# Performance work log

Hardware: AMD Instinct MI355X
Metric: run time of the kernel (lower is better)

Reference implementation:

```python
import jax, jax.numpy as jnp
import numpy as np

N_NODES = 1_000_000
E = 262_144
N_FEAT_COLS = 9        # columns 1..9 of x
CARD = 50_000          # cardinality of each feature embedding table
EMB = 128
EDGE_DIM = 27
# node type (col 0) that activates each feature column h (h = col index - 1):
# files (type 0) use cols 1..4, processes (type 1) use col 5, sockets (type 2) use cols 6..9
TYPE_PER_COL = (0, 0, 0, 0, 1, 2, 2, 2, 2)


def setup_inputs() -> dict:
    key = jax.random.key(0)
    ks = jax.random.split(key, 10)
    type_col = jax.random.randint(ks[0], (N_NODES, 1), 0, 3, dtype=jnp.int32)
    feat_cols = jax.random.randint(ks[1], (N_NODES, N_FEAT_COLS), 0, CARD, dtype=jnp.int32)
    x = jnp.concatenate([type_col, feat_cols], axis=1)  # [N_NODES, 10]
    src = jax.random.randint(ks[2], (E,), 0, N_NODES, dtype=jnp.int32)
    dst = jax.random.randint(ks[3], (E,), 0, N_NODES, dtype=jnp.int32)
    neg_dst = jax.random.randint(ks[4], (E,), 0, N_NODES, dtype=jnp.int32)
    msg = jax.random.normal(ks[5], (E, EDGE_DIM), dtype=jnp.float32)
    emb_type = jax.random.normal(ks[6], (3, EMB), dtype=jnp.float32)            # embeddings[0]
    emb_feats = jax.random.normal(ks[7], (N_FEAT_COLS, CARD, EMB), dtype=jnp.float32)  # embeddings[1..9]
    edge_w = jax.random.normal(ks[8], (EMB, EDGE_DIM), dtype=jnp.float32) / np.sqrt(EDGE_DIM)
    edge_b = jnp.zeros((EMB,), dtype=jnp.float32)
    out_w = jax.random.normal(ks[9], (1, EMB), dtype=jnp.float32) / np.sqrt(EMB)
    out_b = jnp.zeros((1,), dtype=jnp.float32)
    return dict(x=x, src=src, dst=dst, neg_dst=neg_dst, msg=msg,
                emb_type=emb_type, emb_feats=emb_feats,
                edge_w=edge_w, edge_b=edge_b, out_w=out_w, out_b=out_b)


def _encode_features(rows, emb_type, emb_feats):
    """rows: [E,10] int. Equivalent to torch encode_features: per node type,
    sum the type-specific embedding lookups; col-0 (type) embedding is shared."""
    t = rows[:, 0]                     # [E] node type
    out = emb_type[t]                  # embeddings[0] applies to every type
    for h in range(N_FEAT_COLS):       # small fixed loop over 9 tables
        mask = (t == TYPE_PER_COL[h]).astype(out.dtype)[:, None]   # [E,1]
        out = out + emb_feats[h][rows[:, h + 1]] * mask            # masked gather-sum
    return out                         # [E, EMB]


def reference(x, src, dst, neg_dst, msg, emb_type, emb_feats, edge_w, edge_b, out_w, out_b):
    h_src = _encode_features(x[src], emb_type, emb_feats)       # [E, EMB]
    h_pos_dst = _encode_features(x[dst], emb_type, emb_feats)
    h_neg_dst = _encode_features(x[neg_dst], emb_type, emb_feats)
    target_msg = msg @ edge_w.T + edge_b                        # Linear(edge_dim -> EMB)
    h_pos_edge = jax.nn.relu(h_src + h_pos_dst)
    h_neg_edge = jax.nn.relu(h_src + h_neg_dst)
    pos = (h_pos_edge + target_msg) @ out_w.T + out_b           # [E, 1]
    neg = (h_neg_edge + target_msg) @ out_w.T + out_b           # [E, 1]
    return (pos, neg)
```

## Files before the change

### kernel.cpp

```cpp
#include <hip/hip_runtime.h>

#define NUM_EDGES 262144
#define CARD 50000
#define EMB 128
#define EDGE_DIM 27

__global__ void prep_kernel(const float* __restrict__ edge_w,
                            const float* __restrict__ edge_b,
                            const float* __restrict__ out_w,
                            const float* __restrict__ out_b,
                            float* __restrict__ ws) {
    int j = threadIdx.x;
    if (j < EDGE_DIM) {
        float s = 0.f;
        for (int k = 0; k < EMB; ++k) s += out_w[k] * edge_w[k * EDGE_DIM + j];
        ws[j] = s;
    } else if (j == EDGE_DIM) {
        float s = out_b[0];
        for (int k = 0; k < EMB; ++k) s += edge_b[k] * out_w[k];
        ws[EDGE_DIM] = s;
    }
}

__global__ __launch_bounds__(256, 4) void edge_pred_kernel(
    const int* __restrict__ x, const int* __restrict__ src,
    const int* __restrict__ dst, const int* __restrict__ neg_dst,
    const float* __restrict__ msg, const float* __restrict__ emb_type,
    const float* __restrict__ emb_feats, const float* __restrict__ out_w,
    const float* __restrict__ ws, float* __restrict__ out) {
    const int lane = threadIdx.x & 63;
    const int wave = threadIdx.x >> 6;
    const int e0 = __builtin_amdgcn_readfirstlane(blockIdx.x * 8 + wave * 2);

    const int half = lane >> 5;
    const int hl = lane & 31;

    float mterm = 0.f;
    if (hl < EDGE_DIM) {
        mterm = msg[(size_t)(e0 + half) * EDGE_DIM + hl] * ws[hl];
    }

    const int loff = lane * 2;

    int nodes[6];
    nodes[0] = src[e0];     nodes[1] = dst[e0];     nodes[2] = neg_dst[e0];
    nodes[3] = src[e0 + 1]; nodes[4] = dst[e0 + 1]; nodes[5] = neg_dst[e0 + 1];

    float2 v[6][5];
    float wpad[6];

#pragma unroll
    for (int n = 0; n < 6; ++n) {
        const int* xr = x + (size_t)nodes[n] * 10;
        const int t = xr[0];
        const int c1 = xr[1], c2 = xr[2], c3 = xr[3], c4 = xr[4], c5 = xr[5],
                  c6 = xr[6], c7 = xr[7], c8 = xr[8], c9 = xr[9];
        const int i0 = (t == 0) ? c1 : (t == 1) ? c5 : c6;
        const int i1 = (t == 0) ? c2 : (t == 1) ? c5 : c7;
        const int i2 = (t == 0) ? c3 : (t == 1) ? c5 : c8;
        const int i3 = (t == 0) ? c4 : (t == 1) ? c5 : c9;
        const int h0 = (t == 0) ? 0 : (t == 1) ? 4 : 5;
        const int h1 = (t == 0) ? 1 : (t == 1) ? 4 : 6;
        const int h2 = (t == 0) ? 2 : (t == 1) ? 4 : 7;
        const int h3 = (t == 0) ? 3 : (t == 1) ? 4 : 8;
        wpad[n] = (t == 1) ? 0.f : 1.f;

        v[n][0] = *(const float2*)(emb_type + (size_t)t * EMB + loff);
        v[n][1] = *(const float2*)(emb_feats + ((size_t)h0 * CARD + (size_t)i0) * EMB + loff);
        v[n][2] = *(const float2*)(emb_feats + ((size_t)h1 * CARD + (size_t)i1) * EMB + loff);
        v[n][3] = *(const float2*)(emb_feats + ((size_t)h2 * CARD + (size_t)i2) * EMB + loff);
        v[n][4] = *(const float2*)(emb_feats + ((size_t)h3 * CARD + (size_t)i3) * EMB + loff);
    }

    float hx[6], hy[6];
#pragma unroll
    for (int n = 0; n < 6; ++n) {
        const float ax = v[n][0].x + v[n][1].x;
        const float ay = v[n][0].y + v[n][1].y;
        const float bx = v[n][2].x + v[n][3].x + v[n][4].x;
        const float by = v[n][2].y + v[n][3].y + v[n][4].y;
        hx[n] = ax + wpad[n] * bx;
        hy[n] = ay + wpad[n] * by;
    }

    const float2 wv = *(const float2*)(out_w + loff);

    float p0 = fmaxf(hx[0] + hx[1], 0.f) * wv.x + fmaxf(hy[0] + hy[1], 0.f) * wv.y;
    float q0 = fmaxf(hx[0] + hx[2], 0.f) * wv.x + fmaxf(hy[0] + hy[2], 0.f) * wv.y;
    float p1 = fmaxf(hx[3] + hx[4], 0.f) * wv.x + fmaxf(hy[3] + hy[4], 0.f) * wv.y;
    float q1 = fmaxf(hx[3] + hx[5], 0.f) * wv.x + fmaxf(hy[3] + hy[5], 0.f) * wv.y;

    if (half == 0) { p0 += mterm; q0 += mterm; }
    else           { p1 += mterm; q1 += mterm; }

    p0 += __shfl_xor(p0, 32, 64);
    q0 += __shfl_xor(q0, 32, 64);
    p1 += __shfl_xor(p1, 32, 64);
    q1 += __shfl_xor(q1, 32, 64);
    float pz = half ? p1 : p0;
    float qz = half ? q1 : q0;
#pragma unroll
    for (int off = 16; off > 0; off >>= 1) {
        pz += __shfl_xor(pz, off, 64);
        qz += __shfl_xor(qz, off, 64);
    }

    if (hl == 0) {
        const float b2 = ws[EDGE_DIM];
        const int e = e0 + half;
        out[e] = pz + b2;
        out[NUM_EDGES + e] = qz + b2;
    }
}

extern "C" void kernel_launch(void* const* d_in, const int* in_sizes, int n_in,
                              void* d_out, int out_size, void* d_ws, size_t ws_size,
                              hipStream_t stream) {
    const int* x = (const int*)d_in[0];
    const int* src = (const int*)d_in[1];
    const int* dst = (const int*)d_in[2];
    const int* neg_dst = (const int*)d_in[3];
    const float* msg = (const float*)d_in[4];
    const float* emb_type = (const float*)d_in[5];
    const float* emb_feats = (const float*)d_in[6];
    const float* edge_w = (const float*)d_in[7];
    const float* edge_b = (const float*)d_in[8];
    const float* out_w = (const float*)d_in[9];
    const float* out_b = (const float*)d_in[10];
    float* out = (float*)d_out;
    float* ws = (float*)d_ws;

    prep_kernel<<<1, 64, 0, stream>>>(edge_w, edge_b, out_w, out_b, ws);

    const int blocks = NUM_EDGES / 8;
    edge_pred_kernel<<<blocks, 256, 0, stream>>>(x, src, dst, neg_dst, msg,
                                                 emb_type, emb_feats, out_w, ws,
                                                 out);
}
```

Before: 510.4 us.

## Gather embedding rows into LDS via direct global_load_lds, one edge per wave

Each wave now handles a single edge and gathers its 15 embedding rows straight into shared memory with 16-byte global_load_lds transfers, two rows per instruction, before reading them back as float2. The msg load becomes nontemporal and the launch-bounds occupancy hint is dropped, while the grid doubles. The aim is wider, fewer gather instructions with less register pressure. The cost is 32 KB of LDS per block, which may cap occupancy, plus an LDS round trip and twice as many index/x-row loads per wave of work.

```diff
diff --git a/kernel.cpp b/kernel.cpp
--- a/kernel.cpp
+++ b/kernel.cpp
@@ -22,36 +22,32 @@
     }
 }
 
-__global__ __launch_bounds__(256, 4) void edge_pred_kernel(
+__global__ __launch_bounds__(256) void edge_pred_kernel(
     const int* __restrict__ x, const int* __restrict__ src,
     const int* __restrict__ dst, const int* __restrict__ neg_dst,
     const float* __restrict__ msg, const float* __restrict__ emb_type,
     const float* __restrict__ emb_feats, const float* __restrict__ out_w,
     const float* __restrict__ ws, float* __restrict__ out) {
+    __shared__ float lds[4 * 16 * EMB];
+
     const int lane = threadIdx.x & 63;
     const int wave = threadIdx.x >> 6;
-    const int e0 = __builtin_amdgcn_readfirstlane(blockIdx.x * 8 + wave * 2);
-
+    const int e = __builtin_amdgcn_readfirstlane(blockIdx.x * 4 + wave);
     const int half = lane >> 5;
     const int hl = lane & 31;
 
     float mterm = 0.f;
-    if (hl < EDGE_DIM) {
-        mterm = msg[(size_t)(e0 + half) * EDGE_DIM + hl] * ws[hl];
-    }
+    if (lane < EDGE_DIM)
+        mterm = __builtin_nontemporal_load(msg + (size_t)e * EDGE_DIM + lane) * ws[lane];
 
-    const int loff = lane * 2;
+    const int n0 = src[e], n1 = dst[e], n2 = neg_dst[e];
 
-    int nodes[6];
-    nodes[0] = src[e0];     nodes[1] = dst[e0];     nodes[2] = neg_dst[e0];
-    nodes[3] = src[e0 + 1]; nodes[4] = dst[e0 + 1]; nodes[5] = neg_dst[e0 + 1];
-
-    float2 v[6][5];
-    float wpad[6];
-
+    const float* rb[16];
+    float wpad[3];
 #pragma unroll
-    for (int n = 0; n < 6; ++n) {
-        const int* xr = x + (size_t)nodes[n] * 10;
+    for (int n = 0; n < 3; ++n) {
+        const int node = (n == 0) ? n0 : (n == 1) ? n1 : n2;
+        const int* xr = x + (size_t)node * 10;
         const int t = xr[0];
         const int c1 = xr[1], c2 = xr[2], c3 = xr[3], c4 = xr[4], c5 = xr[5],
                   c6 = xr[6], c7 = xr[7], c8 = xr[8], c9 = xr[9];
@@ -65,51 +61,57 @@
         const int h3 = (t == 0) ? 3 : (t == 1) ? 4 : 8;
         wpad[n] = (t == 1) ? 0.f : 1.f;
 
-        v[n][0] = *(const float2*)(emb_type + (size_t)t * EMB + loff);
-        v[n][1] = *(const float2*)(emb_feats + ((size_t)h0 * CARD + (size_t)i0) * EMB + loff);
-        v[n][2] = *(const float2*)(emb_feats + ((size_t)h1 * CARD + (size_t)i1) * EMB + loff);
-        v[n][3] = *(const float2*)(emb_feats + ((size_t)h2 * CARD + (size_t)i2) * EMB + loff);
-        v[n][4] = *(const float2*)(emb_feats + ((size_t)h3 * CARD + (size_t)i3) * EMB + loff);
+        rb[5 * n + 0] = emb_type + (size_t)t * EMB;
+        rb[5 * n + 1] = emb_feats + ((size_t)h0 * CARD + (size_t)i0) * EMB;
+        rb[5 * n + 2] = emb_feats + ((size_t)h1 * CARD + (size_t)i1) * EMB;
+        rb[5 * n + 3] = emb_feats + ((size_t)h2 * CARD + (size_t)i2) * EMB;
+        rb[5 * n + 4] = emb_feats + ((size_t)h3 * CARD + (size_t)i3) * EMB;
+    }
+    rb[15] = emb_type;
+
+    float* wbase = lds + wave * (16 * EMB);
+#pragma unroll
+    for (int k = 0; k < 8; ++k) {
+        const float* ga = rb[2 * k];
+        const float* gb = rb[2 * k + 1];
+        const float* g = (half ? gb : ga) + hl * 4;
+        __builtin_amdgcn_global_load_lds(
+            (const __attribute__((address_space(1))) void*)g,
+            (__attribute__((address_space(3))) void*)(wbase + k * 2 * EMB),
+            16, 0, 0);
     }
 
-    float hx[6], hy[6];
+    __builtin_amdgcn_s_waitcnt(0);
+
+    const float2* rows = (const float2*)wbase;
+    float hx[3], hy[3];
 #pragma unroll
-    for (int n = 0; n < 6; ++n) {
-        const float ax = v[n][0].x + v[n][1].x;
-        const float ay = v[n][0].y + v[n][1].y;
-        const float bx = v[n][2].x + v[n][3].x + v[n][4].x;
-        const float by = v[n][2].y + v[n][3].y + v[n][4].y;
-        hx[n] = ax + wpad[n] * bx;
-        hy[n] = ay + wpad[n] * by;
+    for (int n = 0; n < 3; ++n) {
+        const float2 a0 = rows[(5 * n + 0) * 64 + lane];
+        const float2 a1 = rows[(5 * n + 1) * 64 + lane];
+        const float2 a2 = rows[(5 * n + 2) * 64 + lane];
+        const float2 a3 = rows[(5 * n + 3) * 64 + lane];
+        const float2 a4 = rows[(5 * n + 4) * 64 + lane];
+        const float bx = a2.x + a3.x + a4.x;
+        const float by = a2.y + a3.y + a4.y;
+        hx[n] = a0.x + a1.x + wpad[n] * bx;
+        hy[n] = a0.y + a1.y + wpad[n] * by;
     }
 
-    const float2 wv = *(const float2*)(out_w + loff);
+    const float2 wv = *(const float2*)(out_w + lane * 2);
+    float p = fmaxf(hx[0] + hx[1], 0.f) * wv.x + fmaxf(hy[0] + hy[1], 0.f) * wv.y + mterm;
+    float q = fmaxf(hx[0] + hx[2], 0.f) * wv.x + fmaxf(hy[0] + hy[2], 0.f) * wv.y + mterm;
 
-    float p0 = fmaxf(hx[0] + hx[1], 0.f) * wv.x + fmaxf(hy[0] + hy[1], 0.f) * wv.y;
-    float q0 = fmaxf(hx[0] + hx[2], 0.f) * wv.x + fmaxf(hy[0] + hy[2], 0.f) * wv.y;
-    float p1 = fmaxf(hx[3] + hx[4], 0.f) * wv.x + fmaxf(hy[3] + hy[4], 0.f) * wv.y;
-    float q1 = fmaxf(hx[3] + hx[5], 0.f) * wv.x + fmaxf(hy[3] + hy[5], 0.f) * wv.y;
-
-    if (half == 0) { p0 += mterm; q0 += mterm; }
-    else           { p1 += mterm; q1 += mterm; }
-
-    p0 += __shfl_xor(p0, 32, 64);
-    q0 += __shfl_xor(q0, 32, 64);
-    p1 += __shfl_xor(p1, 32, 64);
-    q1 += __shfl_xor(q1, 32, 64);
-    float pz = half ? p1 : p0;
-    float qz = half ? q1 : q0;
 #pragma unroll
-    for (int off = 16; off > 0; off >>= 1) {
-        pz += __shfl_xor(pz, off, 64);
-        qz += __shfl_xor(qz, off, 64);
+    for (int off = 32; off > 0; off >>= 1) {
+        p += __shfl_xor(p, off, 64);
+        q += __shfl_xor(q, off, 64);
     }
 
-    if (hl == 0) {
+    if (lane == 0) {
         const float b2 = ws[EDGE_DIM];
-        const int e = e0 + half;
-        out[e] = pz + b2;
-        out[NUM_EDGES + e] = qz + b2;
+        out[e] = p + b2;
+        out[NUM_EDGES + e] = q + b2;
     }
 }
 
@@ -132,7 +134,7 @@
 
     prep_kernel<<<1, 64, 0, stream>>>(edge_w, edge_b, out_w, out_b, ws);
 
-    const int blocks = NUM_EDGES / 8;
+    const int blocks = NUM_EDGES / 4;
     edge_pred_kernel<<<blocks, 256, 0, stream>>>(x, src, dst, neg_dst, msg,
                                                  emb_type, emb_feats, out_w, ws,
                                                  out);
```

New measurement: 638.8 us. 1.25x slower.
